# Optimization experiments

Hardware: AMD Instinct MI355X
Metric: run time of the kernel (lower is better)

Reference implementation:

```python
import jax, jax.numpy as jnp
import numpy as np

EPS = 1e-7  # keras.backend.epsilon()
ROUTINGS = 3


def squash(v, axis=-1):
    # scale = ||v||^2 / (1+||v||^2) / sqrt(||v||^2 + eps)
    s2 = jnp.sum(jnp.square(v), axis=axis, keepdims=True)
    return v * (s2 / (1.0 + s2) / jnp.sqrt(s2 + EPS))


def setup_inputs() -> dict:
    key = jax.random.key(0)
    k1, k2 = jax.random.split(key)
    B, I, P = 256, 1152, 8   # batch, primcap_num, primcap_dim
    J, D = 10, 16            # digitcap_num, digitcap_dim
    x = jax.random.normal(k1, (B, I, P), dtype=jnp.float32)
    W = jax.random.normal(k2, (I, J, D, P), dtype=jnp.float32) * 0.01
    return {"x": x, "W": W}


def reference(x, W):
    # votes u_hat[b,i,j,d] = W[i,j,d,:] @ x[b,i,:]  (implicit broadcast, no tiling)
    votes = jnp.einsum('ijdp,bip->bijd', W, x)            # [B,I,J,D]
    B, I, J, _ = votes.shape
    b = jnp.zeros((B, I, J), dtype=votes.dtype)
    v = None
    for r in range(ROUTINGS):
        c = jax.nn.softmax(b, axis=2)                      # over digit capsules
        s = jnp.einsum('bij,bijd->bjd', c, votes)          # weighted sum over prim caps
        v = squash(s, axis=-1)                             # [B,J,D]
        if r < ROUTINGS - 1:
            b = b + jnp.einsum('bijd,bjd->bij', votes, v)  # agreement
    return v
```

## Files before the change

### kernel.cpp

```cpp
#include <hip/hip_runtime.h>
#include <cstdint>
#include <cstddef>

constexpr int Bn = 256, In = 1152, Pn = 8, Jn = 10, Dn = 16;
constexpr int CA = 8, NCH = In / CA;

template <int MASK>
__device__ __forceinline__ float swzadd(float v) {
  const int s = __builtin_amdgcn_ds_swizzle(__float_as_int(v), MASK);
  return v + __int_as_float(s);
}

__device__ __forceinline__ float rowsum16(float v) {
  v = swzadd<0x041F>(v);
  v = swzadd<0x081F>(v);
  v = swzadd<0x101F>(v);
  v = swzadd<0x201F>(v);
  return v;
}

__device__ __forceinline__ float dot8(const float4 a0, const float4 a1,
                                      const float4 b0, const float4 b1) {
  float s = a0.x * b0.x;
  s = fmaf(a0.y, b0.y, s); s = fmaf(a0.z, b0.z, s); s = fmaf(a0.w, b0.w, s);
  s = fmaf(a1.x, b1.x, s); s = fmaf(a1.y, b1.y, s); s = fmaf(a1.z, b1.z, s);
  s = fmaf(a1.w, b1.w, s);
  return s;
}

template <int MODE>
__global__ __launch_bounds__(256)
__attribute__((amdgpu_waves_per_eu(3, 4)))
void capsV(const float* __restrict__ x, const float* __restrict__ w,
           const float* __restrict__ vsumT, float* __restrict__ spart) {
  __shared__ float4 wlds[CA * Jn * 2 * 16];
  const int t = threadIdx.x;
  const int d = t & 15, q = t >> 4;
  const int ch = blockIdx.x;
  const int b0 = blockIdx.y * 32 + q, b1 = b0 + 16;
  const int i0 = ch * CA;

  const float4* wg =
      reinterpret_cast<const float4*>(w + (size_t)i0 * (Jn * Dn * Pn));
  #pragma unroll
  for (int k = 0; k < (CA * Jn * 2 * 16) / 256; ++k) {
    const int g = t + k * 256;
    const int h = g & 1, dd = (g >> 1) & 15, ij = g >> 5;
    wlds[(ij * 2 + h) * 16 + dd] = wg[g];
  }

  float vs0[Jn], vs1[Jn], acc0[Jn], acc1[Jn];
  #pragma unroll
  for (int j = 0; j < Jn; ++j) {
    acc0[j] = 0.f; acc1[j] = 0.f;
    if (MODE) {
      vs0[j] = vsumT[((size_t)j * Bn + b0) * Dn + d];
      vs1[j] = vsumT[((size_t)j * Bn + b1) * Dn + d];
    }
  }

  __syncthreads();

  const float* xp0 = x + ((size_t)b0 * In + i0) * Pn;
  const float* xp1 = x + ((size_t)b1 * In + i0) * Pn;

  for (int ii = 0; ii < CA; ++ii) {
    const float4 xa0 = reinterpret_cast<const float4*>(xp0)[0];
    const float4 xa1 = reinterpret_cast<const float4*>(xp0)[1];
    const float4 xb0 = reinterpret_cast<const float4*>(xp1)[0];
    const float4 xb1 = reinterpret_cast<const float4*>(xp1)[1];

    float vt0[Jn], vt1[Jn];
    #pragma unroll
    for (int j = 0; j < Jn; ++j) {
      const float4* wrow = &wlds[((ii * Jn + j) * 2) * 16 + d];
      const float4 w0 = wrow[0];
      const float4 w1 = wrow[16];
      vt0[j] = dot8(w0, w1, xa0, xa1);
      vt1[j] = dot8(w0, w1, xb0, xb1);
    }

    if (MODE) {
      float l0[Jn], l1[Jn];
      #pragma unroll
      for (int j = 0; j < Jn; ++j) {
        l0[j] = rowsum16(vt0[j] * vs0[j]);
        l1[j] = rowsum16(vt1[j] * vs1[j]);
      }
      float sa = 0.f, sb = 0.f;
      #pragma unroll
      for (int j = 0; j < Jn; ++j) {
        l0[j] = __expf(l0[j]); sa += l0[j];
        l1[j] = __expf(l1[j]); sb += l1[j];
      }
      const float ia = __builtin_amdgcn_rcpf(sa);
      const float ib = __builtin_amdgcn_rcpf(sb);
      #pragma unroll
      for (int j = 0; j < Jn; ++j) {
        acc0[j] = fmaf(l0[j] * ia, vt0[j], acc0[j]);
        acc1[j] = fmaf(l1[j] * ib, vt1[j], acc1[j]);
      }
    } else {
      #pragma unroll
      for (int j = 0; j < Jn; ++j) { acc0[j] += vt0[j]; acc1[j] += vt1[j]; }
    }

    xp0 += Pn;
    xp1 += Pn;
  }

  const float cs = MODE ? 1.f : 0.1f;
  #pragma unroll
  for (int j = 0; j < Jn; ++j) {
    spart[(((size_t)ch * Jn + j) * Bn + b0) * Dn + d] = acc0[j] * cs;
    spart[(((size_t)ch * Jn + j) * Bn + b1) * Dn + d] = acc1[j] * cs;
  }
}

template <int MODE>
__global__ __launch_bounds__(1024) void capsF(
    const float* __restrict__ spart, float* __restrict__ vsumT,
    float* __restrict__ out) {
  __shared__ float red[4][16][16];
  const int t = threadIdx.x;
  const int cg = t >> 8, r = t & 255, g = r >> 4, d = r & 15;
  const int j = blockIdx.x, b = blockIdx.y * 16 + g;

  const size_t cstride = (size_t)Jn * Bn * Dn;
  const size_t cstep = 4 * cstride;
  const float* sp = spart + (((size_t)cg * Jn + j) * Bn + b) * Dn + d;
  float s0 = 0.f, s1 = 0.f;
  #pragma unroll 4
  for (int k = 0; k < NCH / 4; k += 2) {
    s0 += sp[0];
    s1 += sp[cstep];
    sp += 2 * cstep;
  }
  red[cg][g][d] = s0 + s1;
  __syncthreads();
  if (t < 256) {
    const float z = red[0][g][d] + red[1][g][d] + red[2][g][d] + red[3][g][d];
    const float n2 = rowsum16(z * z);
    const float sc = n2 / (1.f + n2) / sqrtf(n2 + 1e-7f);
    const float v = z * sc;
    if (MODE == 2) {
      out[((size_t)b * Jn + j) * Dn + d] = v;
    } else if (MODE == 1) {
      vsumT[((size_t)j * Bn + b) * Dn + d] += v;
    } else {
      vsumT[((size_t)j * Bn + b) * Dn + d] = v;
    }
  }
}

extern "C" void kernel_launch(void* const* d_in, const int* in_sizes, int n_in,
                              void* d_out, int out_size, void* d_ws, size_t ws_size,
                              hipStream_t stream) {
  const float* x = (const float*)d_in[0];
  const float* w = (const float*)d_in[1];
  float* vsumT = (float*)d_ws;
  float* spart = vsumT + (size_t)Jn * Bn * Dn;
  float* out = (float*)d_out;

  const dim3 gV(NCH, Bn / 32), gF(Jn, Bn / 16);

  capsV<0><<<gV, 256, 0, stream>>>(x, w, nullptr, spart);
  capsF<0><<<gF, 1024, 0, stream>>>(spart, vsumT, out);

  capsV<1><<<gV, 256, 0, stream>>>(x, w, vsumT, spart);
  capsF<1><<<gF, 1024, 0, stream>>>(spart, vsumT, out);

  capsV<1><<<gV, 256, 0, stream>>>(x, w, vsumT, spart);
  capsF<2><<<gF, 1024, 0, stream>>>(spart, vsumT, out);
}
```

Baseline: 169.5 us.

## Halve W LDS staging in capsV and widen capsF reduction across chunk groups

capsV now stages only half of the chunk's W (4 capsules) into LDS at a time and reloads the second half midway behind two barriers. This halves shared memory per block and drops the waves_per_eu attribute, aiming for higher occupancy. capsF splits the 144-chunk reduction across 8 thread groups of 8 batches instead of 4 groups of 16, doubling its grid and shortening each thread's serial accumulation. The mid-kernel reload adds synchronisation and exposes global W latency, and the compiler may now allocate registers differently.

```diff
diff --git a/kernel.cpp b/kernel.cpp
--- a/kernel.cpp
+++ b/kernel.cpp
@@ -4,6 +4,7 @@
 
 constexpr int Bn = 256, In = 1152, Pn = 8, Jn = 10, Dn = 16;
 constexpr int CA = 8, NCH = In / CA;
+constexpr int CH2 = CA / 2;
 
 template <int MASK>
 __device__ __forceinline__ float swzadd(float v) {
@@ -29,24 +30,25 @@
 }
 
 template <int MODE>
-__global__ __launch_bounds__(256)
-__attribute__((amdgpu_waves_per_eu(3, 4)))
-void capsV(const float* __restrict__ x, const float* __restrict__ w,
-           const float* __restrict__ vsumT, float* __restrict__ spart) {
-  __shared__ float4 wlds[CA * Jn * 2 * 16];
+__global__ __launch_bounds__(256) void capsV(
+    const float* __restrict__ x, const float* __restrict__ w,
+    const float* __restrict__ vsumT, float* __restrict__ spart) {
+  __shared__ float4 wlds[CH2 * Jn * 2 * 16];
   const int t = threadIdx.x;
   const int d = t & 15, q = t >> 4;
   const int ch = blockIdx.x;
   const int b0 = blockIdx.y * 32 + q, b1 = b0 + 16;
   const int i0 = ch * CA;
 
-  const float4* wg =
-      reinterpret_cast<const float4*>(w + (size_t)i0 * (Jn * Dn * Pn));
-  #pragma unroll
-  for (int k = 0; k < (CA * Jn * 2 * 16) / 256; ++k) {
-    const int g = t + k * 256;
-    const int h = g & 1, dd = (g >> 1) & 15, ij = g >> 5;
-    wlds[(ij * 2 + h) * 16 + dd] = wg[g];
+  {
+    const float4* wg =
+        reinterpret_cast<const float4*>(w + (size_t)i0 * (Jn * Dn * Pn));
+    #pragma unroll
+    for (int k = 0; k < 5; ++k) {
+      const int g = t + k * 256;
+      const int h = g & 1, dd = (g >> 1) & 15, ij = g >> 5;
+      wlds[(ij * 2 + h) * 16 + dd] = wg[g];
+    }
   }
 
   float vs0[Jn], vs1[Jn], acc0[Jn], acc1[Jn];
@@ -59,54 +61,71 @@
     }
   }
 
-  __syncthreads();
-
   const float* xp0 = x + ((size_t)b0 * In + i0) * Pn;
   const float* xp1 = x + ((size_t)b1 * In + i0) * Pn;
 
-  for (int ii = 0; ii < CA; ++ii) {
-    const float4 xa0 = reinterpret_cast<const float4*>(xp0)[0];
-    const float4 xa1 = reinterpret_cast<const float4*>(xp0)[1];
-    const float4 xb0 = reinterpret_cast<const float4*>(xp1)[0];
-    const float4 xb1 = reinterpret_cast<const float4*>(xp1)[1];
+  __syncthreads();
 
-    float vt0[Jn], vt1[Jn];
+  #pragma unroll
+  for (int hh = 0; hh < 2; ++hh) {
     #pragma unroll
-    for (int j = 0; j < Jn; ++j) {
-      const float4* wrow = &wlds[((ii * Jn + j) * 2) * 16 + d];
-      const float4 w0 = wrow[0];
-      const float4 w1 = wrow[16];
-      vt0[j] = dot8(w0, w1, xa0, xa1);
-      vt1[j] = dot8(w0, w1, xb0, xb1);
+    for (int il = 0; il < CH2; ++il) {
+      const float4 xa0 = reinterpret_cast<const float4*>(xp0)[0];
+      const float4 xa1 = reinterpret_cast<const float4*>(xp0)[1];
+      const float4 xb0 = reinterpret_cast<const float4*>(xp1)[0];
+      const float4 xb1 = reinterpret_cast<const float4*>(xp1)[1];
+
+      float vt0[Jn], vt1[Jn];
+      #pragma unroll
+      for (int j = 0; j < Jn; ++j) {
+        const float4* wrow = &wlds[((il * Jn + j) * 2) * 16 + d];
+        const float4 w0 = wrow[0];
+        const float4 w1 = wrow[16];
+        vt0[j] = dot8(w0, w1, xa0, xa1);
+        vt1[j] = dot8(w0, w1, xb0, xb1);
+      }
+
+      if (MODE) {
+        float l0[Jn], l1[Jn];
+        #pragma unroll
+        for (int j = 0; j < Jn; ++j) {
+          l0[j] = rowsum16(vt0[j] * vs0[j]);
+          l1[j] = rowsum16(vt1[j] * vs1[j]);
+        }
+        float sa = 0.f, sb = 0.f;
+        #pragma unroll
+        for (int j = 0; j < Jn; ++j) {
+          l0[j] = __expf(l0[j]); sa += l0[j];
+          l1[j] = __expf(l1[j]); sb += l1[j];
+        }
+        const float ia = __builtin_amdgcn_rcpf(sa);
+        const float ib = __builtin_amdgcn_rcpf(sb);
+        #pragma unroll
+        for (int j = 0; j < Jn; ++j) {
+          acc0[j] = fmaf(l0[j] * ia, vt0[j], acc0[j]);
+          acc1[j] = fmaf(l1[j] * ib, vt1[j], acc1[j]);
+        }
+      } else {
+        #pragma unroll
+        for (int j = 0; j < Jn; ++j) { acc0[j] += vt0[j]; acc1[j] += vt1[j]; }
+      }
+
+      xp0 += Pn;
+      xp1 += Pn;
     }
 
-    if (MODE) {
-      float l0[Jn], l1[Jn];
+    if (hh == 0) {
+      __syncthreads();
+      const float4* wg = reinterpret_cast<const float4*>(
+          w + (size_t)(i0 + CH2) * (Jn * Dn * Pn));
       #pragma unroll
-      for (int j = 0; j < Jn; ++j) {
-        l0[j] = rowsum16(vt0[j] * vs0[j]);
-        l1[j] = rowsum16(vt1[j] * vs1[j]);
+      for (int k = 0; k < 5; ++k) {
+        const int g = t + k * 256;
+        const int h = g & 1, dd = (g >> 1) & 15, ij = g >> 5;
+        wlds[(ij * 2 + h) * 16 + dd] = wg[g];
       }
-      float sa = 0.f, sb = 0.f;
-      #pragma unroll
-      for (int j = 0; j < Jn; ++j) {
-        l0[j] = __expf(l0[j]); sa += l0[j];
-        l1[j] = __expf(l1[j]); sb += l1[j];
-      }
-      const float ia = __builtin_amdgcn_rcpf(sa);
-      const float ib = __builtin_amdgcn_rcpf(sb);
-      #pragma unroll
-      for (int j = 0; j < Jn; ++j) {
-        acc0[j] = fmaf(l0[j] * ia, vt0[j], acc0[j]);
-        acc1[j] = fmaf(l1[j] * ib, vt1[j], acc1[j]);
-      }
-    } else {
-      #pragma unroll
-      for (int j = 0; j < Jn; ++j) { acc0[j] += vt0[j]; acc1[j] += vt1[j]; }
+      __syncthreads();
     }
-
-    xp0 += Pn;
-    xp1 += Pn;
   }
 
   const float cs = MODE ? 1.f : 0.1f;
@@ -121,25 +140,27 @@
 __global__ __launch_bounds__(1024) void capsF(
     const float* __restrict__ spart, float* __restrict__ vsumT,
     float* __restrict__ out) {
-  __shared__ float red[4][16][16];
+  __shared__ float red[8][8][16];
   const int t = threadIdx.x;
-  const int cg = t >> 8, r = t & 255, g = r >> 4, d = r & 15;
-  const int j = blockIdx.x, b = blockIdx.y * 16 + g;
+  const int cg = t >> 7, r = t & 127, g = r >> 4, d = r & 15;
+  const int j = blockIdx.x, b = blockIdx.y * 8 + g;
 
   const size_t cstride = (size_t)Jn * Bn * Dn;
-  const size_t cstep = 4 * cstride;
+  const size_t cstep = 8 * cstride;
   const float* sp = spart + (((size_t)cg * Jn + j) * Bn + b) * Dn + d;
   float s0 = 0.f, s1 = 0.f;
-  #pragma unroll 4
-  for (int k = 0; k < NCH / 4; k += 2) {
+  #pragma unroll 3
+  for (int k = 0; k < NCH / 8; k += 2) {
     s0 += sp[0];
     s1 += sp[cstep];
     sp += 2 * cstep;
   }
   red[cg][g][d] = s0 + s1;
   __syncthreads();
-  if (t < 256) {
-    const float z = red[0][g][d] + red[1][g][d] + red[2][g][d] + red[3][g][d];
+  if (t < 128) {
+    float z = 0.f;
+    #pragma unroll
+    for (int c = 0; c < 8; ++c) z += red[c][g][d];
     const float n2 = rowsum16(z * z);
     const float sc = n2 / (1.f + n2) / sqrtf(n2 + 1e-7f);
     const float v = z * sc;
@@ -162,7 +183,7 @@
   float* spart = vsumT + (size_t)Jn * Bn * Dn;
   float* out = (float*)d_out;
 
-  const dim3 gV(NCH, Bn / 32), gF(Jn, Bn / 16);
+  const dim3 gV(NCH, Bn / 32), gF(Jn, Bn / 8);
 
   capsV<0><<<gV, 256, 0, stream>>>(x, w, nullptr, spart);
   capsF<0><<<gF, 1024, 0, stream>>>(spart, vsumT, out);
```

Measured after the change: 364.9 us. +115.3%, slower.
